# Kernel optimization log

Measured on AMD Instinct MI355X. Metric: run time of the kernel, lower is better.

The kernel has to match this reference:

```python
import jax, jax.numpy as jnp
from jax import lax
import numpy as np

# NOTE: the original module calls an opaque CUDA 'approximate dot-product' conv kernel.
# Its backward uses EXACT conv2d gradients for input/weight, so the reference forward
# math is the exact conv2d the kernel approximates. `approximate` is a learned scalar
# controlling the hardware approximation level; it does not change the exact-math output.

STRIDE = 1
PAD = (1, 1)  # (padH, padW)


def setup_inputs() -> dict:
    key = jax.random.key(0)
    k1, k2, k3 = jax.random.split(key, 3)
    B, Cin, H, W = 32, 128, 56, 56
    Cout, K = 256, 3
    x = jax.random.normal(k1, (B, Cin, H, W), dtype=jnp.float32)
    # weight init: uniform(-1, 1) per reset_parameters
    weight = jax.random.uniform(k2, (Cout, Cin, K, K), dtype=jnp.float32, minval=-1.0, maxval=1.0)
    fan_in = Cin * K * K
    bound = 1.0 / np.sqrt(fan_in)
    bias = jax.random.uniform(k3, (Cout,), dtype=jnp.float32, minval=-bound, maxval=bound)
    approximate = jnp.ones((1,), dtype=jnp.float32)
    return {"x": x, "weight": weight, "bias": bias, "approximate": approximate}


def reference(x, weight, bias, approximate):
    # Exact conv2d, NCHW input, OIHW kernel. `approximate` controls only the
    # hardware approximation level in the original CUDA kernel.
    out = lax.conv_general_dilated(
        x, weight,
        window_strides=(STRIDE, STRIDE),
        padding=((PAD[0], PAD[0]), (PAD[1], PAD[1])),
        dimension_numbers=("NCHW", "OIHW", "NCHW"),
    )
    return out + bias.reshape(1, -1, 1, 1)
```

## Files before the change

### kernel.cpp

```cpp
#include <hip/hip_runtime.h>


typedef __attribute__((ext_vector_type(8))) short short8;
typedef __attribute__((ext_vector_type(4))) float floatx4;

typedef __attribute__((address_space(1))) const void* gas_ptr;
typedef __attribute__((address_space(3))) void* las_ptr;

__device__ static inline void gl2lds16(const void* g, void* l) {
    __builtin_amdgcn_global_load_lds((gas_ptr)g, (las_ptr)l, 16, 0, 0);
}

__device__ static inline float bf2f(unsigned short u) {
    union { unsigned int i; float f; } x; x.i = ((unsigned int)u) << 16; return x.f;
}
__device__ static inline unsigned short f2bf(float f) {
    union { float f; unsigned int i; } x; x.f = f;
    unsigned int r = (x.i + 0x7FFFu + ((x.i >> 16) & 1u)) >> 16;
    return (unsigned short)r;
}

__global__ void detect_dtype(const unsigned int* __restrict__ x,
                             unsigned int* __restrict__ flag) {
    int cnt = 0;
    for (int r = 0; r < 4; ++r) {
        unsigned int w = x[r * 64 + threadIdx.x];
        unsigned short lo = (unsigned short)(w & 0xFFFFu);
        int e = (lo >> 7) & 0xFF;
        bool plaus = (lo == 0) || (e >= 96 && e <= 144);
        unsigned long long b = __ballot(plaus);
        if (threadIdx.x == 0) cnt += (int)__popcll(b);
    }
    if (threadIdx.x == 0) *flag = (cnt >= 205) ? 1u : 0u;
}

__global__ void wt_repack(const void* __restrict__ wsrc,
                          unsigned short* __restrict__ wt,
                          const unsigned int* __restrict__ flag) {
    const bool isbf = (*flag != 0);
    int idx = blockIdx.x * 256 + threadIdx.x;
    int ci  = idx & 127;
    int co  = (idx >> 7) & 255;
    int off = idx >> 15;
    size_t s = (size_t)(co * 128 + ci) * 9 + off;
    float v = isbf ? bf2f(((const unsigned short*)wsrc)[s])
                   : ((const float*)wsrc)[s];
    wt[idx] = f2bf(v);
}

__global__ __launch_bounds__(256) void x_repack(
    const void* __restrict__ xsrc, unsigned short* __restrict__ xp,
    const unsigned int* __restrict__ flag) {
    __shared__ unsigned short tile[56 * 130];
    const bool isbf = (*flag != 0);
    const int bh  = blockIdx.x;
    const int b   = bh / 58, hp = bh - b * 58;
    const int tid = threadIdx.x;
    unsigned short* row = xp + (size_t)(b * 58 + hp) * 58 * 128;
    if (hp == 0 || hp == 57) {
        uint4 z; z.x = z.y = z.z = z.w = 0u;
        uint4* r = (uint4*)row;
        for (int t = tid; t < 928; t += 256) r[t] = z;
        return;
    }
    const int h = hp - 1;
    if (isbf) {
        const unsigned short* xs =
            (const unsigned short*)xsrc + (size_t)b * 128 * 3136 + h * 56;
#pragma unroll
        for (int it = 0; it < 7; ++it) {
            int idx = it * 256 + tid;
            int ci = idx / 14, w4 = idx - ci * 14;
            ushort4 v = *(const ushort4*)(xs + (size_t)ci * 3136 + w4 * 4);
            tile[(w4 * 4 + 0) * 130 + ci] = v.x;
            tile[(w4 * 4 + 1) * 130 + ci] = v.y;
            tile[(w4 * 4 + 2) * 130 + ci] = v.z;
            tile[(w4 * 4 + 3) * 130 + ci] = v.w;
        }
    } else {
        const float* xs = (const float*)xsrc + (size_t)b * 128 * 3136 + h * 56;
#pragma unroll
        for (int it = 0; it < 7; ++it) {
            int idx = it * 256 + tid;
            int ci = idx / 14, w4 = idx - ci * 14;
            float4 v = *(const float4*)(xs + (size_t)ci * 3136 + w4 * 4);
            tile[(w4 * 4 + 0) * 130 + ci] = f2bf(v.x);
            tile[(w4 * 4 + 1) * 130 + ci] = f2bf(v.y);
            tile[(w4 * 4 + 2) * 130 + ci] = f2bf(v.z);
            tile[(w4 * 4 + 3) * 130 + ci] = f2bf(v.w);
        }
    }
    __syncthreads();
#pragma unroll
    for (int it = 0; it < 4; ++it) {
        int k = it * 256 + tid;
        if (k >= 928) break;
        int wq = k >> 4, cc = k & 15;
        uint4 v;
        if (wq == 0 || wq == 57) { v.x = v.y = v.z = v.w = 0u; }
        else {
            const unsigned short* p = &tile[(wq - 1) * 130 + cc * 8];
            union { unsigned short s[8]; uint4 u; } pk;
#pragma unroll
            for (int j = 0; j < 8; ++j) pk.s[j] = p[j];
            v = pk.u;
        }
        *(uint4*)(row + wq * 128 + cc * 8) = v;
    }
}

__global__ __launch_bounds__(256) void conv_mfma(
    const unsigned short* __restrict__ xp,
    const unsigned short* __restrict__ wt,
    const void* __restrict__ bias,
    void* __restrict__ out,
    const unsigned int* __restrict__ flag)
{
    __shared__ __align__(16) char lds[32768];
    const bool isbf = (*flag != 0);
    const int tid   = threadIdx.x;
    const int lane  = tid & 63;
    const int wv    = tid >> 6;
    const int ntile = blockIdx.x;
    const int mtile = blockIdx.y;

    const int srow  = wv * 8 + (lane >> 3);
    const int cphys = lane & 7;
    const int clog  = cphys ^ (srow & 7);

    const unsigned short* aBase = wt + (mtile * 128 + srow) * 128 + clog * 8;

    size_t bOff[4];
#pragma unroll
    for (int i = 0; i < 4; ++i) {
        const int n = ntile * 128 + i * 32 + srow;
        const int b = n / 3136, s = n - b * 3136;
        const int h = s / 56,   w = s - h * 56;
        bOff[i] = ((size_t)(b * 58 + h) * 58 + w) * 128 + clog * 8;
    }

    const int mbase = (wv >> 1) * 64 + (lane & 15);
    const int nbase = (wv & 1) * 64 + (lane & 15);
    const int q     = lane >> 4;
    const int rx    = lane & 7;
    const char* la = lds;
    const char* lb = lds + 16384;

    floatx4 acc[4][4] = {};

    for (int step = 0; step < 18; ++step) {
        const int off = step >> 1;
        const int kb  = (step & 1) << 6;
        const int dh  = off / 3, dw = off - dh * 3;
        const int aoff = off * 32768 + kb;
        const size_t boff = (size_t)(dh * 58 + dw) * 128 + kb;
#pragma unroll
        for (int i = 0; i < 4; ++i) {
            gl2lds16(aBase + i * 4096 + aoff, lds + i * 4096 + wv * 1024);
            gl2lds16(xp + bOff[i] + boff, lds + 16384 + i * 4096 + wv * 1024);
        }
        __syncthreads();

#pragma unroll
        for (int s = 0; s < 2; ++s) {
            const int pc = ((s * 4 + q) ^ rx) * 16;
            short8 af[4], bfr[4];
#pragma unroll
            for (int t = 0; t < 4; ++t) {
                af[t]  = *(const short8*)(la + (mbase + t * 16) * 128 + pc);
                bfr[t] = *(const short8*)(lb + (nbase + t * 16) * 128 + pc);
            }
#pragma unroll
            for (int i = 0; i < 4; ++i)
#pragma unroll
                for (int j = 0; j < 4; ++j)
                    acc[i][j] = __builtin_amdgcn_mfma_f32_16x16x32_bf16(
                        af[i], bfr[j], acc[i][j], 0, 0, 0);
        }
        __syncthreads();
    }

#pragma unroll
    for (int j = 0; j < 4; ++j) {
        const int n = ntile * 128 + (wv & 1) * 64 + j * 16 + (lane & 15);
        const int b = n / 3136;
        const int s = n - b * 3136;
#pragma unroll
        for (int i = 0; i < 4; ++i) {
            const int co = mtile * 128 + (wv >> 1) * 64 + i * 16 + q * 4;
            float bv[4];
            if (isbf) {
                const ushort4 bb = *(const ushort4*)((const unsigned short*)bias + co);
                bv[0] = bf2f(bb.x); bv[1] = bf2f(bb.y);
                bv[2] = bf2f(bb.z); bv[3] = bf2f(bb.w);
            } else {
                const float4 bb = *(const float4*)((const float*)bias + co);
                bv[0] = bb.x; bv[1] = bb.y; bv[2] = bb.z; bv[3] = bb.w;
            }
#pragma unroll
            for (int r = 0; r < 4; ++r) {
                const float v = acc[i][j][r] + bv[r];
                const size_t o = (size_t)b * 802816 + (size_t)(co + r) * 3136 + s;
                if (isbf) ((unsigned short*)out)[o] = f2bf(v);
                else      ((float*)out)[o] = v;
            }
        }
    }
}

__global__ void conv_naive(const float* __restrict__ x,
                           const float* __restrict__ w,
                           const float* __restrict__ bias,
                           float* __restrict__ out) {
    long long i = (long long)blockIdx.x * 256 + threadIdx.x;
    if (i >= 25690112LL) return;
    int wo = (int)(i % 56); long long t = i / 56;
    int ho = (int)(t % 56); t /= 56;
    int co = (int)(t % 256); int b = (int)(t / 256);
    float acc = bias[co];
    for (int ci = 0; ci < 128; ++ci)
        for (int dh = 0; dh < 3; ++dh) {
            int hi = ho + dh - 1; if ((unsigned)hi >= 56u) continue;
            for (int dw = 0; dw < 3; ++dw) {
                int wi = wo + dw - 1; if ((unsigned)wi >= 56u) continue;
                acc += x[((size_t)(b * 128 + ci) * 56 + hi) * 56 + wi] *
                       w[((co * 128 + ci) * 3 + dh) * 3 + dw];
            }
        }
    out[i] = acc;
}

extern "C" void kernel_launch(void* const* d_in, const int* in_sizes, int n_in,
                              void* d_out, int out_size, void* d_ws, size_t ws_size,
                              hipStream_t stream) {
    const void* x    = d_in[0];
    const void* w    = d_in[1];
    const void* bias = d_in[2];

    const size_t xp_bytes = (size_t)32 * 58 * 58 * 128 * 2;
    const size_t wt_off   = xp_bytes;
    const size_t wt_bytes = (size_t)9 * 256 * 128 * 2;
    const size_t fl_off   = wt_off + wt_bytes;
    const size_t need     = fl_off + 64;

    if (ws_size >= need) {
        unsigned short* xp = (unsigned short*)d_ws;
        unsigned short* wt = (unsigned short*)((char*)d_ws + wt_off);
        unsigned int* flag = (unsigned int*)((char*)d_ws + fl_off);
        detect_dtype<<<1, 64, 0, stream>>>((const unsigned int*)x, flag);
        x_repack<<<32 * 58, 256, 0, stream>>>(x, xp, flag);
        wt_repack<<<1152, 256, 0, stream>>>(w, wt, flag);
        dim3 grid(784, 2, 1);
        conv_mfma<<<grid, 256, 0, stream>>>(xp, wt, bias, d_out, flag);
    } else {
        conv_naive<<<(25690112 + 255) / 256, 256, 0, stream>>>(
            (const float*)x, (const float*)w, (const float*)bias, (float*)d_out);
    }
}
```

Baseline: 232.5 us.

## Warp-specialize conv into producer/consumer waves with 4-stage LDS ring

Adds two producer wavefronts that stream weight and input tiles into a four-buffer LDS ring using global_load_lds. Four consumer wavefronts spin on per-buffer ready/freed counters instead of block-wide barriers. The K-step is halved to 32 and the swizzle is changed to suit the narrower rows. The aim is to overlap global loads with MFMA work and remove the __syncthreads stalls. In exchange it doubles LDS use to 64KB, which cuts blocks per CU, and relies on spin-wait correctness, including waitcnt semantics for LDS-direct loads.

Measured after the change: 244.3 us. 5.1% more time.

```diff
diff --git a/kernel.cpp b/kernel.cpp
--- a/kernel.cpp
+++ b/kernel.cpp
@@ -109,14 +109,16 @@
     }
 }
 
-__global__ __launch_bounds__(256) void conv_mfma(
+__global__ __launch_bounds__(384) void conv_mfma(
     const unsigned short* __restrict__ xp,
     const unsigned short* __restrict__ wt,
     const void* __restrict__ bias,
     void* __restrict__ out,
     const unsigned int* __restrict__ flag)
 {
-    __shared__ __align__(16) char lds[32768];
+    __shared__ __align__(16) char lds[65536];
+    __shared__ unsigned ready[4];
+    __shared__ unsigned freed[4];
     const bool isbf = (*flag != 0);
     const int tid   = threadIdx.x;
     const int lane  = tid & 63;
@@ -124,62 +126,80 @@
     const int ntile = blockIdx.x;
     const int mtile = blockIdx.y;
 
-    const int srow  = wv * 8 + (lane >> 3);
-    const int cphys = lane & 7;
-    const int clog  = cphys ^ (srow & 7);
-
-    const unsigned short* aBase = wt + (mtile * 128 + srow) * 128 + clog * 8;
-
-    size_t bOff[4];
-#pragma unroll
-    for (int i = 0; i < 4; ++i) {
-        const int n = ntile * 128 + i * 32 + srow;
-        const int b = n / 3136, s = n - b * 3136;
-        const int h = s / 56,   w = s - h * 56;
-        bOff[i] = ((size_t)(b * 58 + h) * 58 + w) * 128 + clog * 8;
+    if (tid < 4) { ready[tid] = 0u; freed[tid] = 0u; }
+    __syncthreads();
+
+    if (wv >= 4) {
+        const int pid = wv - 4;
+        const int srp = lane >> 2;
+        const int clg = (lane & 3) ^ ((lane >> 3) & 3);
+        const unsigned short* aB = wt + (mtile * 128 + srp) * 128 + clg * 8;
+        size_t bRow[8];
+#pragma unroll
+        for (int i = 0; i < 8; ++i) {
+            const int n = ntile * 128 + i * 16 + srp;
+            const int b = n / 3136, s2 = n - b * 3136;
+            const int h = s2 / 56,  w = s2 - h * 56;
+            bRow[i] = ((size_t)(b * 58 + h) * 58 + w) * 128 + clg * 8;
+        }
+        for (int s = pid; s < 36; s += 2) {
+            const int bf_ = s & 3, cyc = s >> 2;
+            if (cyc > 0) {
+                const unsigned gate = 4u * (unsigned)cyc;
+                while (__hip_atomic_load(&freed[bf_], __ATOMIC_ACQUIRE,
+                                         __HIP_MEMORY_SCOPE_WORKGROUP) < gate)
+                    __builtin_amdgcn_s_sleep(1);
+            }
+            char* buf = lds + bf_ * 16384;
+            const int off = s >> 2, kb = (s & 3) << 5;
+            const int dh = off / 3, dw = off - dh * 3;
+            const int aoff = off * 32768 + kb;
+            const int boff = (dh * 58 + dw) * 128 + kb;
+#pragma unroll
+            for (int i = 0; i < 8; ++i)
+                gl2lds16(aB + i * 2048 + aoff, buf + i * 1024);
+#pragma unroll
+            for (int i = 0; i < 8; ++i)
+                gl2lds16(xp + bRow[i] + boff, buf + 8192 + i * 1024);
+            __builtin_amdgcn_s_waitcnt(0x3F70);
+            if (lane == 0)
+                __hip_atomic_store(&ready[bf_], (unsigned)(s + 1),
+                                   __ATOMIC_RELEASE, __HIP_MEMORY_SCOPE_WORKGROUP);
+        }
+        return;
     }
 
     const int mbase = (wv >> 1) * 64 + (lane & 15);
     const int nbase = (wv & 1) * 64 + (lane & 15);
-    const int q     = lane >> 4;
-    const int rx    = lane & 7;
-    const char* la = lds;
-    const char* lb = lds + 16384;
-
+    const int ph    = (lane >> 4) ^ (((lane & 15) >> 1) & 3);
     floatx4 acc[4][4] = {};
 
-    for (int step = 0; step < 18; ++step) {
-        const int off = step >> 1;
-        const int kb  = (step & 1) << 6;
-        const int dh  = off / 3, dw = off - dh * 3;
-        const int aoff = off * 32768 + kb;
-        const size_t boff = (size_t)(dh * 58 + dw) * 128 + kb;
-#pragma unroll
-        for (int i = 0; i < 4; ++i) {
-            gl2lds16(aBase + i * 4096 + aoff, lds + i * 4096 + wv * 1024);
-            gl2lds16(xp + bOff[i] + boff, lds + 16384 + i * 4096 + wv * 1024);
-        }
-        __syncthreads();
-
-#pragma unroll
-        for (int s = 0; s < 2; ++s) {
-            const int pc = ((s * 4 + q) ^ rx) * 16;
-            short8 af[4], bfr[4];
-#pragma unroll
-            for (int t = 0; t < 4; ++t) {
-                af[t]  = *(const short8*)(la + (mbase + t * 16) * 128 + pc);
-                bfr[t] = *(const short8*)(lb + (nbase + t * 16) * 128 + pc);
-            }
-#pragma unroll
-            for (int i = 0; i < 4; ++i)
-#pragma unroll
-                for (int j = 0; j < 4; ++j)
-                    acc[i][j] = __builtin_amdgcn_mfma_f32_16x16x32_bf16(
-                        af[i], bfr[j], acc[i][j], 0, 0, 0);
-        }
-        __syncthreads();
-    }
-
+#pragma unroll 4
+    for (int s = 0; s < 36; ++s) {
+        const int bf_ = s & 3;
+        while (__hip_atomic_load(&ready[bf_], __ATOMIC_ACQUIRE,
+                                 __HIP_MEMORY_SCOPE_WORKGROUP) < (unsigned)(s + 1))
+            ;
+        const char* la = lds + bf_ * 16384;
+        const char* lb = la + 8192;
+        short8 af[4], bfr[4];
+#pragma unroll
+        for (int t = 0; t < 4; ++t) {
+            af[t]  = *(const short8*)(la + (mbase + t * 16) * 64 + ph * 16);
+            bfr[t] = *(const short8*)(lb + (nbase + t * 16) * 64 + ph * 16);
+        }
+#pragma unroll
+        for (int i = 0; i < 4; ++i)
+#pragma unroll
+            for (int j = 0; j < 4; ++j)
+                acc[i][j] = __builtin_amdgcn_mfma_f32_16x16x32_bf16(
+                    af[i], bfr[j], acc[i][j], 0, 0, 0);
+        if (lane == 0)
+            __hip_atomic_fetch_add(&freed[bf_], 1u, __ATOMIC_RELEASE,
+                                   __HIP_MEMORY_SCOPE_WORKGROUP);
+    }
+
+    const int q = lane >> 4;
 #pragma unroll
     for (int j = 0; j < 4; ++j) {
         const int n = ntile * 128 + (wv & 1) * 64 + j * 16 + (lane & 15);
@@ -251,7 +271,7 @@
         x_repack<<<32 * 58, 256, 0, stream>>>(x, xp, flag);
         wt_repack<<<1152, 256, 0, stream>>>(w, wt, flag);
         dim3 grid(784, 2, 1);
-        conv_mfma<<<grid, 256, 0, stream>>>(xp, wt, bias, d_out, flag);
+        conv_mfma<<<grid, 384, 0, stream>>>(xp, wt, bias, d_out, flag);
     } else {
         conv_naive<<<(25690112 + 255) / 256, 256, 0, stream>>>(
             (const float*)x, (const float*)w, (const float*)bias, (float*)d_out);
```
